# Optimization experiments

Hardware: AMD Instinct MI355X
Metric: run time of the kernel (lower is better)

Reference implementation:

```python
import jax, jax.numpy as jnp
import numpy as np

B, S, D, H = 4, 2048, 1024, 16
DK = D // H


def setup_inputs() -> dict:
    key = jax.random.key(0)
    ks = jax.random.split(key, 7)
    xq = jax.random.normal(ks[0], (B, S, D), dtype=jnp.float32)
    xk = jax.random.normal(ks[1], (B, S, D), dtype=jnp.float32)
    xv = jax.random.normal(ks[2], (B, S, D), dtype=jnp.float32)
    attention_mask = jnp.ones((B, S), dtype=jnp.int32)  # all-valid padding mask
    scale = 0.02
    Wq = jax.random.normal(ks[3], (D, D), dtype=jnp.float32) * scale
    Wk = jax.random.normal(ks[4], (D, D), dtype=jnp.float32) * scale
    Wv = jax.random.normal(ks[5], (D, D), dtype=jnp.float32) * scale
    Wo = jax.random.normal(ks[6], (D, D), dtype=jnp.float32) * scale
    return {"x_query": xq, "x_key": xk, "x_value": xv,
            "attention_mask": attention_mask,
            "Wq": Wq, "Wk": Wk, "Wv": Wv, "Wo": Wo}


def reference(x_query, x_key, x_value, attention_mask, Wq, Wk, Wv, Wo):
    b, sq, d = x_query.shape
    sk = x_key.shape[1]
    # nn.Linear(bias=False): y = x @ W.T
    Q = x_query @ Wq.T
    K = x_key @ Wk.T
    V = x_value @ Wv.T
    # torch .split(dk, dim=-1) -> contiguous head slices == reshape (B,S,H,DK)
    Qh = Q.reshape(b, sq, H, DK).transpose(0, 2, 1, 3)  # (B,H,Sq,DK)
    Kh = K.reshape(b, sk, H, DK).transpose(0, 2, 1, 3)
    Vh = V.reshape(b, sk, H, DK).transpose(0, 2, 1, 3)
    scores = jnp.einsum('bhqd,bhkd->bhqk', Qh, Kh) / jnp.sqrt(
        jnp.asarray(DK, dtype=Qh.dtype))
    # causal mask (mask_future=True)
    causal = jnp.tril(jnp.ones((sq, sk), dtype=bool))
    scores = jnp.where(causal[None, None, :, :], scores, -jnp.inf)
    # padding mask (B,Sk) -> (B,1,1,Sk)
    pad = (attention_mask != 0)[:, None, None, :]
    scores = jnp.where(pad, scores, -jnp.inf)
    attn = jax.nn.softmax(scores, axis=-1)
    out = jnp.einsum('bhqk,bhkd->bhqd', attn, Vh)  # (B,H,Sq,DK)
    out = out.transpose(0, 2, 1, 3).reshape(b, sq, d)
    return out @ Wo.T
```

## Files before the change

kernel.cpp:

```cpp
#include <hip/hip_runtime.h>
#include <stdint.h>

#define BB 4
#define SS 2048
#define DD 1024
#define HH 16
#define DKK 64

typedef unsigned short u16;
typedef short s16x8 __attribute__((ext_vector_type(8)));
typedef float f32x4 __attribute__((ext_vector_type(4)));

__device__ __forceinline__ void async_copy16(const void* g, void* l) {
  __builtin_amdgcn_global_load_lds(
      (const __attribute__((address_space(1))) void*)g,
      (__attribute__((address_space(3))) void*)l, 16, 0, 0);
}

__device__ __forceinline__ u16 f2bf(float f) {
  union { float f; uint32_t u; } x; x.f = f;
  uint32_t r = x.u + 0x7fffu + ((x.u >> 16) & 1u);
  return (u16)(r >> 16);
}

__device__ __forceinline__ uint32_t cvtpk(float a, float b) {
  uint32_t d;
  asm("v_cvt_pk_bf16_f32 %0, %1, %2" : "=v"(d) : "v"(a), "v"(b));
  return d;
}

__device__ __forceinline__ uint32_t swz16(uint32_t x) {
  return (uint32_t)__builtin_amdgcn_ds_swizzle((int)x, 0x401F);
}

__global__ __launch_bounds__(256) void cvt_kernel(
    const float* __restrict__ x0, const float* __restrict__ x1,
    const float* __restrict__ x2, const float* __restrict__ w0,
    const float* __restrict__ w1, const float* __restrict__ w2,
    const float* __restrict__ w3, u16* __restrict__ dst) {
  const size_t base = ((size_t)blockIdx.x * 256 + threadIdx.x) * 8;
  const float* src;
  size_t off;
  if (base < 25165824ull) {
    const size_t t = base >> 23;
    src = (t == 0) ? x0 : (t == 1) ? x1 : x2;
    off = base & 8388607ull;
  } else {
    const size_t r = base - 25165824ull;
    const size_t t = r >> 20;
    src = (t == 0) ? w0 : (t == 1) ? w1 : (t == 2) ? w2 : w3;
    off = r & 1048575ull;
  }
  const float4 a = *(const float4*)(src + off);
  const float4 b = *(const float4*)(src + off + 4);
  s16x8 o;
  o[0] = (short)f2bf(a.x); o[1] = (short)f2bf(a.y);
  o[2] = (short)f2bf(a.z); o[3] = (short)f2bf(a.w);
  o[4] = (short)f2bf(b.x); o[5] = (short)f2bf(b.y);
  o[6] = (short)f2bf(b.z); o[7] = (short)f2bf(b.w);
  *(s16x8*)(dst + base) = o;
}

template <bool IN_F32, bool OUT_F32>
__global__ __launch_bounds__(256, 3) void gemm_bt(
    const void* __restrict__ Ap, const void* __restrict__ Bp, void* __restrict__ Cp,
    size_t asegstride, size_t bsegstride, size_t csegstride, int vt_seg) {
  const int K = 1024, N = 1024;
  __shared__ u16 Alds[128 * 64];
  __shared__ u16 Blds[128 * 64];
  const int tid = threadIdx.x;
  const int wid = tid >> 6, lane = tid & 63;
  const int quad = lane >> 4, l16 = lane & 15;
  const int mtile = blockIdx.x >> 3;
  const int ntile = blockIdx.x & 7;
  const int wm = wid >> 1, wn = wid & 1;
  const int seg = blockIdx.y;
  f32x4 acc[4][4] = {};
  for (int kb = 0; kb < K; kb += 64) {
    if constexpr (IN_F32) {
      const float* Af = (const float*)Ap + seg * asegstride + (size_t)mtile * 128 * K;
      const float* Bf = (const float*)Bp + seg * bsegstride + (size_t)ntile * 128 * K;
#pragma unroll
      for (int i = 0; i < 8; ++i) {
        const int c = i * 256 + tid;
        const int row = c >> 4, g = c & 15;
        const int cc = g >> 1, h = g & 1;
        const int sl = row * 8 + (cc ^ (row & 7));
        {
          const float4 v = *(const float4*)(Af + (size_t)row * K + kb + g * 4);
          ushort4 o;
          o.x = f2bf(v.x); o.y = f2bf(v.y); o.z = f2bf(v.z); o.w = f2bf(v.w);
          *(ushort4*)&Alds[sl * 8 + h * 4] = o;
        }
        {
          const float4 v = *(const float4*)(Bf + (size_t)row * K + kb + g * 4);
          ushort4 o;
          o.x = f2bf(v.x); o.y = f2bf(v.y); o.z = f2bf(v.z); o.w = f2bf(v.w);
          *(ushort4*)&Blds[sl * 8 + h * 4] = o;
        }
      }
    } else {
      const u16* Ab = (const u16*)Ap + seg * asegstride + (size_t)mtile * 128 * K;
      const u16* Bb = (const u16*)Bp + seg * bsegstride + (size_t)ntile * 128 * K;
#pragma unroll
      for (int i = 0; i < 4; ++i) {
        const int s = i * 256 + tid;
        const int row = s >> 3;
        const int cc = (s & 7) ^ (row & 7);
        async_copy16(Ab + (size_t)row * K + kb + cc * 8,
                     (char*)Alds + (i * 256 + wid * 64) * 16);
        async_copy16(Bb + (size_t)row * K + kb + cc * 8,
                     (char*)Blds + (i * 256 + wid * 64) * 16);
      }
    }
    __syncthreads();
#pragma unroll
    for (int ks = 0; ks < 2; ++ks) {
      s16x8 af[4], bfr[4];
#pragma unroll
      for (int i = 0; i < 4; ++i) {
        const int R = wm * 64 + i * 16 + l16;
        af[i] = *(const s16x8*)&Alds[(R * 8 + ((ks * 4 + quad) ^ (l16 & 7))) * 8];
      }
#pragma unroll
      for (int j = 0; j < 4; ++j) {
        const int R = wn * 64 + j * 16 + l16;
        bfr[j] = *(const s16x8*)&Blds[(R * 8 + ((ks * 4 + quad) ^ (l16 & 7))) * 8];
      }
#pragma unroll
      for (int i = 0; i < 4; ++i)
#pragma unroll
        for (int j = 0; j < 4; ++j)
          acc[i][j] = __builtin_amdgcn_mfma_f32_16x16x32_bf16(af[i], bfr[j], acc[i][j], 0, 0, 0);
    }
    __syncthreads();
  }
  const int row0 = mtile * 128 + wm * 64 + quad * 4;
  const int col0 = ntile * 128 + wn * 64 + l16;
  if (seg == vt_seg) {
    u16* VT = (u16*)Cp + (size_t)seg * csegstride;
#pragma unroll
    for (int i = 0; i < 4; ++i)
#pragma unroll
      for (int j = 0; j < 4; ++j) {
        const int col = col0 + j * 16;
        const int row = row0 + i * 16;
        const int bb = row >> 11, s0 = row & 2047;
        const size_t dst = (((size_t)bb * HH + (col >> 6)) * DKK + (col & 63)) * SS + s0;
        ushort4 o;
        o.x = f2bf(acc[i][j][0]); o.y = f2bf(acc[i][j][1]);
        o.z = f2bf(acc[i][j][2]); o.w = f2bf(acc[i][j][3]);
        *(ushort4*)(VT + dst) = o;
      }
  } else {
#pragma unroll
    for (int i = 0; i < 4; ++i)
#pragma unroll
      for (int j = 0; j < 4; ++j)
#pragma unroll
        for (int r = 0; r < 4; ++r) {
          const size_t idx = (size_t)(row0 + i * 16 + r) * N + col0 + j * 16;
          if constexpr (OUT_F32) ((float*)Cp)[seg * csegstride + idx] = acc[i][j][r];
          else                   ((u16*)Cp)[seg * csegstride + idx] = f2bf(acc[i][j][r]);
        }
  }
}

__global__ __launch_bounds__(256, 4) void attn_kernel(
    const u16* __restrict__ Q, const u16* __restrict__ K, const u16* __restrict__ VT,
    const int* __restrict__ mask, u16* __restrict__ O) {
  __shared__ u16 Klds[64 * 64];
  __shared__ u16 Vt[64 * 64];
  __shared__ float bias[64];
  const int bid = blockIdx.x;
  const int qt = 15 - (bid >> 6);
  const int b = (bid >> 4) & 3;
  const int h = bid & 15;
  const int tid = threadIdx.x;
  const int wid = tid >> 6, lane = tid & 63;
  const int quad = lane >> 4, l16 = lane & 15;
  const int q0 = qt * 128;
  const u16* Qb = Q + ((size_t)b * SS + q0) * DD + h * DKK;
  const u16* Kb0 = K + (size_t)b * SS * DD + h * DKK;
  const u16* VTb = VT + ((size_t)(b * HH + h)) * DKK * SS;
  s16x8 qf[2][2];
#pragma unroll
  for (int rg = 0; rg < 2; ++rg)
#pragma unroll
    for (int ks = 0; ks < 2; ++ks)
      qf[rg][ks] = *(const s16x8*)(Qb + (size_t)(wid * 32 + rg * 16 + l16) * DD +
                                   ks * 32 + quad * 8);
  s16x8 onesf;
#pragma unroll
  for (int i = 0; i < 8; ++i) onesf[i] = (short)0x3F80;
  f32x4 oacc[2][4] = {};
  f32x4 lacc[2] = {};
  const float c_scale = 0.18033688f;
  const bool qodd = (quad & 1) != 0;
  const bool is_hi = (lane >= 32);
  const bool midq = (quad == 1) || (quad == 2);
  const int xaddr = (lane ^ 32) << 2;
  const int qrow0 = q0 + wid * 32 + l16;
  auto mixf = [&](uint32_t vj0, uint32_t vj1) -> uint32_t {
    const uint32_t S  = is_hi ? vj1 : vj0;
    const uint32_t S2 = is_hi ? vj0 : vj1;
    const uint32_t R  = (uint32_t)__builtin_amdgcn_ds_bpermute(xaddr, (int)S2);
    return midq ? R : S;
  };
  const int ktiles = 2 * qt + 2;
  for (int kt = 0; kt < ktiles; ++kt) {
    const u16* Kb = Kb0 + (size_t)(kt * 64) * DD;
#pragma unroll
    for (int i = 0; i < 2; ++i) {
      const int s = i * 256 + tid;
      const int row = s >> 3;
      const int cc = (s & 7) ^ (row & 7);
      async_copy16(Kb + (size_t)row * DD + cc * 8,
                   (char*)Klds + (i * 256 + wid * 64) * 16);
    }
#pragma unroll
    for (int i = 0; i < 2; ++i) {
      const int s = i * 256 + tid;
      const int row = s >> 3;
      const int cc = (s & 7) ^ (row & 7);
      async_copy16(VTb + (size_t)row * SS + kt * 64 + cc * 8,
                   (char*)Vt + ((i * 256 + wid * 64) * 16));
    }
    if (tid < 64) bias[tid] = mask[(size_t)b * SS + kt * 64 + tid] ? 0.0f : -1e30f;
    __syncthreads();
    f32x4 bj[4];
#pragma unroll
    for (int j = 0; j < 4; ++j) bj[j] = *(const f32x4*)&bias[j * 16 + quad * 4];
    f32x4 st[2][4] = {};
#pragma unroll
    for (int ks = 0; ks < 2; ++ks) {
      s16x8 kf[4];
#pragma unroll
      for (int j = 0; j < 4; ++j) {
        const int R = j * 16 + l16;
        kf[j] = *(const s16x8*)&Klds[(R * 8 + ((ks * 4 + quad) ^ (l16 & 7))) * 8];
      }
#pragma unroll
      for (int rg = 0; rg < 2; ++rg)
#pragma unroll
        for (int j = 0; j < 4; ++j)
          st[rg][j] = __builtin_amdgcn_mfma_f32_16x16x32_bf16(kf[j], qf[rg][ks],
                                                              st[rg][j], 0, 0, 0);
    }
    const bool causal = (kt >= 2 * qt);
    uint32_t pkv[2][8];
#pragma unroll
    for (int rg = 0; rg < 2; ++rg) {
      const int qrow = qrow0 + rg * 16;
#pragma unroll
      for (int j = 0; j < 4; ++j) {
        float p[4];
#pragma unroll
        for (int r = 0; r < 4; ++r) {
          float v = __builtin_amdgcn_exp2f(st[rg][j][r] * c_scale + bj[j][r]);
          if (causal && (kt * 64 + j * 16 + quad * 4 + r) > qrow) v = 0.0f;
          p[r] = v;
        }
        pkv[rg][j * 2 + 0] = cvtpk(p[0], p[1]);
        pkv[rg][j * 2 + 1] = cvtpk(p[2], p[3]);
      }
    }
#pragma unroll
    for (int ks = 0; ks < 2; ++ks) {
      const int j0 = ks * 2, j1 = ks * 2 + 1;
      s16x8 pf[2];
#pragma unroll
      for (int rg = 0; rg < 2; ++rg) {
        const uint32_t Xa0 = pkv[rg][j0 * 2 + 0], Xa1 = pkv[rg][j0 * 2 + 1];
        const uint32_t Xb0 = pkv[rg][j1 * 2 + 0], Xb1 = pkv[rg][j1 * 2 + 1];
        const uint32_t Pa0 = swz16(Xa0), Pa1 = swz16(Xa1);
        const uint32_t Pb0 = swz16(Xb0), Pb1 = swz16(Xb1);
        const uint32_t Ea0 = qodd ? Pa0 : Xa0, Oa0 = qodd ? Xa0 : Pa0;
        const uint32_t Ea1 = qodd ? Pa1 : Xa1, Oa1 = qodd ? Xa1 : Pa1;
        const uint32_t Eb0 = qodd ? Pb0 : Xb0, Ob0 = qodd ? Xb0 : Pb0;
        const uint32_t Eb1 = qodd ? Pb1 : Xb1, Ob1 = qodd ? Xb1 : Pb1;
        union { uint32_t w[4]; s16x8 v; } u;
        u.w[0] = mixf(Ea0, Eb0);
        u.w[1] = mixf(Ea1, Eb1);
        u.w[2] = mixf(Oa0, Ob0);
        u.w[3] = mixf(Oa1, Ob1);
        pf[rg] = u.v;
      }
#pragma unroll
      for (int jt = 0; jt < 4; ++jt) {
        const int d = jt * 16 + l16;
        const s16x8 vf = *(const s16x8*)&Vt[(d * 8 + ((ks * 4 + quad) ^ (d & 7))) * 8];
#pragma unroll
        for (int rg = 0; rg < 2; ++rg)
          oacc[rg][jt] = __builtin_amdgcn_mfma_f32_16x16x32_bf16(pf[rg], vf,
                                                                oacc[rg][jt], 0, 0, 0);
      }
#pragma unroll
      for (int rg = 0; rg < 2; ++rg)
        lacc[rg] = __builtin_amdgcn_mfma_f32_16x16x32_bf16(pf[rg], onesf, lacc[rg],
                                                           0, 0, 0);
    }
    __syncthreads();
  }
  u16* Ob = O + ((size_t)b * SS + q0) * DD + h * DKK;
#pragma unroll
  for (int rg = 0; rg < 2; ++rg)
#pragma unroll
    for (int r = 0; r < 4; ++r) {
      const float inv = 1.0f / lacc[rg][r];
      const int row = wid * 32 + rg * 16 + quad * 4 + r;
#pragma unroll
      for (int jt = 0; jt < 4; ++jt)
        Ob[(size_t)row * DD + jt * 16 + l16] = f2bf(oacc[rg][jt][r] * inv);
    }
}

extern "C" void kernel_launch(void* const* d_in, const int* in_sizes, int n_in,
                              void* d_out, int out_size, void* d_ws, size_t ws_size,
                              hipStream_t stream) {
  const float* xq = (const float*)d_in[0];
  const float* xk = (const float*)d_in[1];
  const float* xv = (const float*)d_in[2];
  const int* mask = (const int*)d_in[3];
  const float* Wq = (const float*)d_in[4];
  const float* Wk = (const float*)d_in[5];
  const float* Wv = (const float*)d_in[6];
  const float* Wo = (const float*)d_in[7];
  float* out = (float*)d_out;
  const size_t elems = (size_t)BB * SS * DD;
  const size_t welems = (size_t)DD * DD;
  if (ws_size >= 109051904ull) {
    u16* wsb = (u16*)d_ws;
    u16* Xq = wsb;
    u16* Wqb = wsb + 3 * elems;
    u16* Wob = Wqb + 3 * welems;
    u16* Qb = wsb + 3 * elems + 4 * welems;
    u16* Kb = Qb + elems;
    u16* Vb = Kb + elems;
    u16* Ob = wsb;
    cvt_kernel<<<14336, 256, 0, stream>>>(xq, xk, xv, Wq, Wk, Wv, Wo, wsb);
    gemm_bt<false, false><<<dim3(512, 3), 256, 0, stream>>>(
        Xq, Wqb, Qb, elems, welems, elems, 2);
    attn_kernel<<<BB * HH * (SS / 128), 256, 0, stream>>>(Qb, Kb, Vb, mask, Ob);
    gemm_bt<false, true><<<dim3(512, 1), 256, 0, stream>>>(Ob, Wob, out, 0, 0, 0, -1);
  } else {
    u16* Qb = (u16*)d_ws;
    u16* Kb = Qb + elems;
    u16* Vb = Kb + elems;
    u16* Ob = Vb + elems;
    gemm_bt<true, false><<<dim3(512, 1), 256, 0, stream>>>(xq, Wq, Qb, 0, 0, 0, -1);
    gemm_bt<true, false><<<dim3(512, 1), 256, 0, stream>>>(xk, Wk, Kb, 0, 0, 0, -1);
    gemm_bt<true, false><<<dim3(512, 1), 256, 0, stream>>>(xv, Wv, Vb, 0, 0, 0, 0);
    attn_kernel<<<BB * HH * (SS / 128), 256, 0, stream>>>(Qb, Kb, Vb, mask, Ob);
    gemm_bt<false, true><<<dim3(512, 1), 256, 0, stream>>>(Ob, Wo, out, 0, 0, 0, -1);
  }
}
```

Before: 318.4 us.

## Pair causal query tiles per attention block and swizzle GEMM tile order

The attention kernel now runs 512-thread blocks over 256-row query tiles. Each block handles two complementary tiles (qt and 7-qt), so every block does about the same amount of causal work, and only 256 blocks are launched. Each K/V tile loaded into LDS is shared by 8 waves instead of 4. Separately, the GEMM block index is swizzled to change the order in which M/N tiles are visited, which changes cache reuse. The trade-off is fewer, larger blocks: lower occupancy and only one wave of blocks across the CUs.

```diff
diff --git a/kernel.cpp b/kernel.cpp
--- a/kernel.cpp
+++ b/kernel.cpp
@@ -71,8 +71,10 @@
   const int tid = threadIdx.x;
   const int wid = tid >> 6, lane = tid & 63;
   const int quad = lane >> 4, l16 = lane & 15;
-  const int mtile = blockIdx.x >> 3;
-  const int ntile = blockIdx.x & 7;
+  const int bidx = blockIdx.x;
+  const int swz = ((bidx & 7) << 6) | (bidx >> 3);
+  const int mtile = swz >> 3;
+  const int ntile = swz & 7;
   const int wm = wid >> 1, wn = wid & 1;
   const int seg = blockIdx.y;
   f32x4 acc[4][4] = {};
@@ -166,153 +168,146 @@
   }
 }
 
-__global__ __launch_bounds__(256, 4) void attn_kernel(
+__global__ __launch_bounds__(512, 2) void attn_kernel(
     const u16* __restrict__ Q, const u16* __restrict__ K, const u16* __restrict__ VT,
     const int* __restrict__ mask, u16* __restrict__ O) {
   __shared__ u16 Klds[64 * 64];
   __shared__ u16 Vt[64 * 64];
   __shared__ float bias[64];
   const int bid = blockIdx.x;
-  const int qt = 15 - (bid >> 6);
+  const int pairidx = bid >> 6;
   const int b = (bid >> 4) & 3;
   const int h = bid & 15;
   const int tid = threadIdx.x;
   const int wid = tid >> 6, lane = tid & 63;
   const int quad = lane >> 4, l16 = lane & 15;
-  const int q0 = qt * 128;
-  const u16* Qb = Q + ((size_t)b * SS + q0) * DD + h * DKK;
   const u16* Kb0 = K + (size_t)b * SS * DD + h * DKK;
   const u16* VTb = VT + ((size_t)(b * HH + h)) * DKK * SS;
-  s16x8 qf[2][2];
-#pragma unroll
-  for (int rg = 0; rg < 2; ++rg)
-#pragma unroll
-    for (int ks = 0; ks < 2; ++ks)
-      qf[rg][ks] = *(const s16x8*)(Qb + (size_t)(wid * 32 + rg * 16 + l16) * DD +
-                                   ks * 32 + quad * 8);
   s16x8 onesf;
 #pragma unroll
   for (int i = 0; i < 8; ++i) onesf[i] = (short)0x3F80;
-  f32x4 oacc[2][4] = {};
-  f32x4 lacc[2] = {};
   const float c_scale = 0.18033688f;
   const bool qodd = (quad & 1) != 0;
   const bool is_hi = (lane >= 32);
   const bool midq = (quad == 1) || (quad == 2);
   const int xaddr = (lane ^ 32) << 2;
-  const int qrow0 = q0 + wid * 32 + l16;
   auto mixf = [&](uint32_t vj0, uint32_t vj1) -> uint32_t {
     const uint32_t S  = is_hi ? vj1 : vj0;
     const uint32_t S2 = is_hi ? vj0 : vj1;
     const uint32_t R  = (uint32_t)__builtin_amdgcn_ds_bpermute(xaddr, (int)S2);
     return midq ? R : S;
   };
-  const int ktiles = 2 * qt + 2;
-  for (int kt = 0; kt < ktiles; ++kt) {
-    const u16* Kb = Kb0 + (size_t)(kt * 64) * DD;
-#pragma unroll
-    for (int i = 0; i < 2; ++i) {
-      const int s = i * 256 + tid;
-      const int row = s >> 3;
-      const int cc = (s & 7) ^ (row & 7);
-      async_copy16(Kb + (size_t)row * DD + cc * 8,
-                   (char*)Klds + (i * 256 + wid * 64) * 16);
+  const int srow = tid >> 3;
+  const int scc = (tid & 7) ^ (srow & 7);
+
+  for (int half = 0; half < 2; ++half) {
+    const int qt = half ? pairidx : (7 - pairidx);
+    const int q0 = qt * 256;
+    const u16* Qb = Q + ((size_t)b * SS + q0) * DD + h * DKK;
+    s16x8 qf[2][2];
+#pragma unroll
+    for (int rg = 0; rg < 2; ++rg)
+#pragma unroll
+      for (int ks = 0; ks < 2; ++ks)
+        qf[rg][ks] = *(const s16x8*)(Qb + (size_t)(wid * 32 + rg * 16 + l16) * DD +
+                                     ks * 32 + quad * 8);
+    f32x4 oacc[2][4] = {};
+    f32x4 lacc[2] = {};
+    const int qrow0 = q0 + wid * 32 + l16;
+    const int ktiles = 4 * qt + 4;
+    for (int kt = 0; kt < ktiles; ++kt) {
+      async_copy16(Kb0 + (size_t)(kt * 64 + srow) * DD + scc * 8,
+                   (char*)Klds + wid * 1024);
+      async_copy16(VTb + (size_t)srow * SS + kt * 64 + scc * 8,
+                   (char*)Vt + wid * 1024);
+      if (tid < 64) bias[tid] = mask[(size_t)b * SS + kt * 64 + tid] ? 0.0f : -1e30f;
+      __syncthreads();
+      f32x4 bj[4];
+#pragma unroll
+      for (int j = 0; j < 4; ++j) bj[j] = *(const f32x4*)&bias[j * 16 + quad * 4];
+      f32x4 st[2][4] = {};
+#pragma unroll
+      for (int ks = 0; ks < 2; ++ks) {
+        s16x8 kf[4];
+#pragma unroll
+        for (int j = 0; j < 4; ++j) {
+          const int R = j * 16 + l16;
+          kf[j] = *(const s16x8*)&Klds[(R * 8 + ((ks * 4 + quad) ^ (l16 & 7))) * 8];
+        }
+#pragma unroll
+        for (int rg = 0; rg < 2; ++rg)
+#pragma unroll
+          for (int j = 0; j < 4; ++j)
+            st[rg][j] = __builtin_amdgcn_mfma_f32_16x16x32_bf16(kf[j], qf[rg][ks],
+                                                                st[rg][j], 0, 0, 0);
+      }
+      const bool causal = (kt >= 4 * qt);
+      uint32_t pkv[2][8];
+#pragma unroll
+      for (int rg = 0; rg < 2; ++rg) {
+        const int qrow = qrow0 + rg * 16;
+#pragma unroll
+        for (int j = 0; j < 4; ++j) {
+          float p[4];
+#pragma unroll
+          for (int r = 0; r < 4; ++r) {
+            float v = __builtin_amdgcn_exp2f(st[rg][j][r] * c_scale + bj[j][r]);
+            if (causal && (kt * 64 + j * 16 + quad * 4 + r) > qrow) v = 0.0f;
+            p[r] = v;
+          }
+          pkv[rg][j * 2 + 0] = cvtpk(p[0], p[1]);
+          pkv[rg][j * 2 + 1] = cvtpk(p[2], p[3]);
+        }
+      }
+#pragma unroll
+      for (int ks = 0; ks < 2; ++ks) {
+        const int j0 = ks * 2, j1 = ks * 2 + 1;
+        s16x8 pf[2];
+#pragma unroll
+        for (int rg = 0; rg < 2; ++rg) {
+          const uint32_t Xa0 = pkv[rg][j0 * 2 + 0], Xa1 = pkv[rg][j0 * 2 + 1];
+          const uint32_t Xb0 = pkv[rg][j1 * 2 + 0], Xb1 = pkv[rg][j1 * 2 + 1];
+          const uint32_t Pa0 = swz16(Xa0), Pa1 = swz16(Xa1);
+          const uint32_t Pb0 = swz16(Xb0), Pb1 = swz16(Xb1);
+          const uint32_t Ea0 = qodd ? Pa0 : Xa0, Oa0 = qodd ? Xa0 : Pa0;
+          const uint32_t Ea1 = qodd ? Pa1 : Xa1, Oa1 = qodd ? Xa1 : Pa1;
+          const uint32_t Eb0 = qodd ? Pb0 : Xb0, Ob0 = qodd ? Xb0 : Pb0;
+          const uint32_t Eb1 = qodd ? Pb1 : Xb1, Ob1 = qodd ? Xb1 : Pb1;
+          union { uint32_t w[4]; s16x8 v; } u;
+          u.w[0] = mixf(Ea0, Eb0);
+          u.w[1] = mixf(Ea1, Eb1);
+          u.w[2] = mixf(Oa0, Ob0);
+          u.w[3] = mixf(Oa1, Ob1);
+          pf[rg] = u.v;
+        }
+#pragma unroll
+        for (int jt = 0; jt < 4; ++jt) {
+          const int d = jt * 16 + l16;
+          const s16x8 vf = *(const s16x8*)&Vt[(d * 8 + ((ks * 4 + quad) ^ (d & 7))) * 8];
+#pragma unroll
+          for (int rg = 0; rg < 2; ++rg)
+            oacc[rg][jt] = __builtin_amdgcn_mfma_f32_16x16x32_bf16(pf[rg], vf,
+                                                                  oacc[rg][jt], 0, 0, 0);
+        }
+#pragma unroll
+        for (int rg = 0; rg < 2; ++rg)
+          lacc[rg] = __builtin_amdgcn_mfma_f32_16x16x32_bf16(pf[rg], onesf, lacc[rg],
+                                                             0, 0, 0);
+      }
+      __syncthreads();
     }
-#pragma unroll
-    for (int i = 0; i < 2; ++i) {
-      const int s = i * 256 + tid;
-      const int row = s >> 3;
-      const int cc = (s & 7) ^ (row & 7);
-      async_copy16(VTb + (size_t)row * SS + kt * 64 + cc * 8,
-                   (char*)Vt + ((i * 256 + wid * 64) * 16));
-    }
-    if (tid < 64) bias[tid] = mask[(size_t)b * SS + kt * 64 + tid] ? 0.0f : -1e30f;
-    __syncthreads();
-    f32x4 bj[4];
-#pragma unroll
-    for (int j = 0; j < 4; ++j) bj[j] = *(const f32x4*)&bias[j * 16 + quad * 4];
-    f32x4 st[2][4] = {};
-#pragma unroll
-    for (int ks = 0; ks < 2; ++ks) {
-      s16x8 kf[4];
-#pragma unroll
-      for (int j = 0; j < 4; ++j) {
-        const int R = j * 16 + l16;
-        kf[j] = *(const s16x8*)&Klds[(R * 8 + ((ks * 4 + quad) ^ (l16 & 7))) * 8];
-      }
-#pragma unroll
-      for (int rg = 0; rg < 2; ++rg)
-#pragma unroll
-        for (int j = 0; j < 4; ++j)
-          st[rg][j] = __builtin_amdgcn_mfma_f32_16x16x32_bf16(kf[j], qf[rg][ks],
-                                                              st[rg][j], 0, 0, 0);
-    }
-    const bool causal = (kt >= 2 * qt);
-    uint32_t pkv[2][8];
-#pragma unroll
-    for (int rg = 0; rg < 2; ++rg) {
-      const int qrow = qrow0 + rg * 16;
-#pragma unroll
-      for (int j = 0; j < 4; ++j) {
-        float p[4];
-#pragma unroll
-        for (int r = 0; r < 4; ++r) {
-          float v = __builtin_amdgcn_exp2f(st[rg][j][r] * c_scale + bj[j][r]);
-          if (causal && (kt * 64 + j * 16 + quad * 4 + r) > qrow) v = 0.0f;
-          p[r] = v;
-        }
-        pkv[rg][j * 2 + 0] = cvtpk(p[0], p[1]);
-        pkv[rg][j * 2 + 1] = cvtpk(p[2], p[3]);
-      }
-    }
-#pragma unroll
-    for (int ks = 0; ks < 2; ++ks) {
-      const int j0 = ks * 2, j1 = ks * 2 + 1;
-      s16x8 pf[2];
-#pragma unroll
-      for (int rg = 0; rg < 2; ++rg) {
-        const uint32_t Xa0 = pkv[rg][j0 * 2 + 0], Xa1 = pkv[rg][j0 * 2 + 1];
-        const uint32_t Xb0 = pkv[rg][j1 * 2 + 0], Xb1 = pkv[rg][j1 * 2 + 1];
-        const uint32_t Pa0 = swz16(Xa0), Pa1 = swz16(Xa1);
-        const uint32_t Pb0 = swz16(Xb0), Pb1 = swz16(Xb1);
-        const uint32_t Ea0 = qodd ? Pa0 : Xa0, Oa0 = qodd ? Xa0 : Pa0;
-        const uint32_t Ea1 = qodd ? Pa1 : Xa1, Oa1 = qodd ? Xa1 : Pa1;
-        const uint32_t Eb0 = qodd ? Pb0 : Xb0, Ob0 = qodd ? Xb0 : Pb0;
-        const uint32_t Eb1 = qodd ? Pb1 : Xb1, Ob1 = qodd ? Xb1 : Pb1;
-        union { uint32_t w[4]; s16x8 v; } u;
-        u.w[0] = mixf(Ea0, Eb0);
-        u.w[1] = mixf(Ea1, Eb1);
-        u.w[2] = mixf(Oa0, Ob0);
-        u.w[3] = mixf(Oa1, Ob1);
-        pf[rg] = u.v;
-      }
-#pragma unroll
-      for (int jt = 0; jt < 4; ++jt) {
-        const int d = jt * 16 + l16;
-        const s16x8 vf = *(const s16x8*)&Vt[(d * 8 + ((ks * 4 + quad) ^ (d & 7))) * 8];
-#pragma unroll
-        for (int rg = 0; rg < 2; ++rg)
-          oacc[rg][jt] = __builtin_amdgcn_mfma_f32_16x16x32_bf16(pf[rg], vf,
-                                                                oacc[rg][jt], 0, 0, 0);
-      }
-#pragma unroll
-      for (int rg = 0; rg < 2; ++rg)
-        lacc[rg] = __builtin_amdgcn_mfma_f32_16x16x32_bf16(pf[rg], onesf, lacc[rg],
-                                                           0, 0, 0);
-    }
-    __syncthreads();
-  }
-  u16* Ob = O + ((size_t)b * SS + q0) * DD + h * DKK;
-#pragma unroll
-  for (int rg = 0; rg < 2; ++rg)
-#pragma unroll
-    for (int r = 0; r < 4; ++r) {
-      const float inv = 1.0f / lacc[rg][r];
-      const int row = wid * 32 + rg * 16 + quad * 4 + r;
-#pragma unroll
-      for (int jt = 0; jt < 4; ++jt)
-        Ob[(size_t)row * DD + jt * 16 + l16] = f2bf(oacc[rg][jt][r] * inv);
-    }
+    u16* Ob = O + ((size_t)b * SS + q0) * DD + h * DKK;
+#pragma unroll
+    for (int rg = 0; rg < 2; ++rg)
+#pragma unroll
+      for (int r = 0; r < 4; ++r) {
+        const float inv = 1.0f / lacc[rg][r];
+        const int row = wid * 32 + rg * 16 + quad * 4 + r;
+#pragma unroll
+        for (int jt = 0; jt < 4; ++jt)
+          Ob[(size_t)row * DD + jt * 16 + l16] = f2bf(oacc[rg][jt][r] * inv);
+      }
+  }
 }
 
 extern "C" void kernel_launch(void* const* d_in, const int* in_sizes, int n_in,
@@ -341,7 +336,7 @@
     cvt_kernel<<<14336, 256, 0, stream>>>(xq, xk, xv, Wq, Wk, Wv, Wo, wsb);
     gemm_bt<false, false><<<dim3(512, 3), 256, 0, stream>>>(
         Xq, Wqb, Qb, elems, welems, elems, 2);
-    attn_kernel<<<BB * HH * (SS / 128), 256, 0, stream>>>(Qb, Kb, Vb, mask, Ob);
+    attn_kernel<<<256, 512, 0, stream>>>(Qb, Kb, Vb, mask, Ob);
     gemm_bt<false, true><<<dim3(512, 1), 256, 0, stream>>>(Ob, Wob, out, 0, 0, 0, -1);
   } else {
     u16* Qb = (u16*)d_ws;
@@ -351,7 +346,7 @@
     gemm_bt<true, false><<<dim3(512, 1), 256, 0, stream>>>(xq, Wq, Qb, 0, 0, 0, -1);
     gemm_bt<true, false><<<dim3(512, 1), 256, 0, stream>>>(xk, Wk, Kb, 0, 0, 0, -1);
     gemm_bt<true, false><<<dim3(512, 1), 256, 0, stream>>>(xv, Wv, Vb, 0, 0, 0, 0);
-    attn_kernel<<<BB * HH * (SS / 128), 256, 0, stream>>>(Qb, Kb, Vb, mask, Ob);
+    attn_kernel<<<256, 512, 0, stream>>>(Qb, Kb, Vb, mask, Ob);
     gemm_bt<false, true><<<dim3(512, 1), 256, 0, stream>>>(Ob, Wo, out, 0, 0, 0, -1);
   }
 }
```

After: 324.3 us. No clear change (+1.9%).

## Split long causal attention tiles across two blocks and add combine kernel

Applied to the files above, without the earlier changes.

The causal attention launch gets a split-K mode. The eight longest query tiles per (batch, head) are split into two halves over the key range, each writing fp32 partial outputs and row sums, and a new combine kernel merges them. The block-to-tile mapping is a hard-coded schedule meant to balance work across the 1536 blocks. This targets the load imbalance from causal triangles and adds extra fp32 traffic plus one more launch. The GEMM block index is also swizzled, changing the order in which tiles are visited for cache locality.

```diff
diff --git a/kernel.cpp b/kernel.cpp
--- a/kernel.cpp
+++ b/kernel.cpp
@@ -71,8 +71,10 @@
   const int tid = threadIdx.x;
   const int wid = tid >> 6, lane = tid & 63;
   const int quad = lane >> 4, l16 = lane & 15;
-  const int mtile = blockIdx.x >> 3;
-  const int ntile = blockIdx.x & 7;
+  const int bidx = blockIdx.x;
+  const int swz = ((bidx & 7) << 6) | (bidx >> 3);
+  const int mtile = swz >> 3;
+  const int ntile = swz & 7;
   const int wm = wid >> 1, wn = wid & 1;
   const int seg = blockIdx.y;
   f32x4 acc[4][4] = {};
@@ -166,16 +168,35 @@
   }
 }
 
+template <int MODE>
 __global__ __launch_bounds__(256, 4) void attn_kernel(
     const u16* __restrict__ Q, const u16* __restrict__ K, const u16* __restrict__ VT,
-    const int* __restrict__ mask, u16* __restrict__ O) {
+    const int* __restrict__ mask, u16* __restrict__ O,
+    float* __restrict__ Opart, float* __restrict__ lpart) {
   __shared__ u16 Klds[64 * 64];
   __shared__ u16 Vt[64 * 64];
   __shared__ float bias[64];
   const int bid = blockIdx.x;
-  const int qt = 15 - (bid >> 6);
-  const int b = (bid >> 4) & 3;
-  const int h = bid & 15;
+  int qt, kt0, kt1, code, bh;
+  if constexpr (MODE == 0) {
+    qt = 15 - (bid >> 6);
+    bh = bid & 63;
+    code = 2;
+    kt0 = 0; kt1 = 2 * qt + 2;
+  } else {
+    bh = bid & 63;
+    const int w = bid >> 6;
+    const int wsel = w >> 3, wo = w & 7;
+    const uint32_t qw = (wsel == 0) ? 0xDD6EE7FFu : (wsel == 1) ? 0x4AABB5CCu : 0x01238899u;
+    const uint32_t sw = (wsel == 0) ? 0x4924u : (wsel == 1) ? 0x9124u : 0xAA44u;
+    qt = (int)((qw >> (wo * 4)) & 15u);
+    code = (int)((sw >> (wo * 2)) & 3u);
+    const int half = qt + 1;
+    kt0 = (code == 1) ? half : 0;
+    kt1 = (code == 0) ? half : 2 * qt + 2;
+  }
+  const int b = bh >> 4;
+  const int h = bh & 15;
   const int tid = threadIdx.x;
   const int wid = tid >> 6, lane = tid & 63;
   const int quad = lane >> 4, l16 = lane & 15;
@@ -207,8 +228,7 @@
     const uint32_t R  = (uint32_t)__builtin_amdgcn_ds_bpermute(xaddr, (int)S2);
     return midq ? R : S;
   };
-  const int ktiles = 2 * qt + 2;
-  for (int kt = 0; kt < ktiles; ++kt) {
+  for (int kt = kt0; kt < kt1; ++kt) {
     const u16* Kb = Kb0 + (size_t)(kt * 64) * DD;
 #pragma unroll
     for (int i = 0; i < 2; ++i) {
@@ -302,17 +322,61 @@
     }
     __syncthreads();
   }
-  u16* Ob = O + ((size_t)b * SS + q0) * DD + h * DKK;
-#pragma unroll
-  for (int rg = 0; rg < 2; ++rg)
-#pragma unroll
-    for (int r = 0; r < 4; ++r) {
-      const float inv = 1.0f / lacc[rg][r];
-      const int row = wid * 32 + rg * 16 + quad * 4 + r;
-#pragma unroll
-      for (int jt = 0; jt < 4; ++jt)
-        Ob[(size_t)row * DD + jt * 16 + l16] = f2bf(oacc[rg][jt][r] * inv);
-    }
+  if (code == 2) {
+    u16* Ob = O + ((size_t)b * SS + q0) * DD + h * DKK;
+#pragma unroll
+    for (int rg = 0; rg < 2; ++rg)
+#pragma unroll
+      for (int r = 0; r < 4; ++r) {
+        const float inv = 1.0f / lacc[rg][r];
+        const int row = wid * 32 + rg * 16 + quad * 4 + r;
+#pragma unroll
+        for (int jt = 0; jt < 4; ++jt)
+          Ob[(size_t)row * DD + jt * 16 + l16] = f2bf(oacc[rg][jt][r] * inv);
+      }
+  } else {
+    const int tile = (bh << 3) + (qt - 8);
+    const int p = tile * 2 + code;
+    float* Op = Opart + (size_t)p * 8192;
+    float* lp = lpart + (size_t)p * 128;
+#pragma unroll
+    for (int rg = 0; rg < 2; ++rg)
+#pragma unroll
+      for (int r = 0; r < 4; ++r) {
+        const int row = wid * 32 + rg * 16 + quad * 4 + r;
+        if (l16 == 0) lp[row] = lacc[rg][r];
+#pragma unroll
+        for (int jt = 0; jt < 4; ++jt)
+          Op[row * 64 + jt * 16 + l16] = oacc[rg][jt][r];
+      }
+  }
+}
+
+__global__ __launch_bounds__(256) void combine_kernel(
+    const float* __restrict__ Opart, const float* __restrict__ lpart,
+    u16* __restrict__ O) {
+  const int tile = blockIdx.x;
+  const int bh = tile >> 3;
+  const int qt = (tile & 7) + 8;
+  const int b = bh >> 4, h = bh & 15;
+  const int tid = threadIdx.x;
+  const int row = tid >> 1;
+  const int c0 = (tid & 1) * 32;
+  const float* P0 = Opart + ((size_t)tile * 2 + 0) * 8192 + row * 64 + c0;
+  const float* P1 = Opart + ((size_t)tile * 2 + 1) * 8192 + row * 64 + c0;
+  const float l = lpart[((size_t)tile * 2 + 0) * 128 + row] +
+                  lpart[((size_t)tile * 2 + 1) * 128 + row];
+  const float inv = 1.0f / l;
+  u16* Ob = O + ((size_t)b * SS + qt * 128 + row) * DD + h * DKK + c0;
+#pragma unroll
+  for (int i = 0; i < 8; ++i) {
+    const f32x4 a = *(const f32x4*)(P0 + i * 4);
+    const f32x4 c = *(const f32x4*)(P1 + i * 4);
+    ushort4 o;
+    o.x = f2bf((a[0] + c[0]) * inv); o.y = f2bf((a[1] + c[1]) * inv);
+    o.z = f2bf((a[2] + c[2]) * inv); o.w = f2bf((a[3] + c[3]) * inv);
+    *(ushort4*)(Ob + i * 4) = o;
+  }
 }
 
 extern "C" void kernel_launch(void* const* d_in, const int* in_sizes, int n_in,
@@ -338,10 +402,13 @@
     u16* Kb = Qb + elems;
     u16* Vb = Kb + elems;
     u16* Ob = wsb;
+    float* Opart = (float*)(wsb + elems);
+    float* lpart = (float*)(wsb + 3 * elems);
     cvt_kernel<<<14336, 256, 0, stream>>>(xq, xk, xv, Wq, Wk, Wv, Wo, wsb);
     gemm_bt<false, false><<<dim3(512, 3), 256, 0, stream>>>(
         Xq, Wqb, Qb, elems, welems, elems, 2);
-    attn_kernel<<<BB * HH * (SS / 128), 256, 0, stream>>>(Qb, Kb, Vb, mask, Ob);
+    attn_kernel<1><<<1536, 256, 0, stream>>>(Qb, Kb, Vb, mask, Ob, Opart, lpart);
+    combine_kernel<<<512, 256, 0, stream>>>(Opart, lpart, Ob);
     gemm_bt<false, true><<<dim3(512, 1), 256, 0, stream>>>(Ob, Wob, out, 0, 0, 0, -1);
   } else {
     u16* Qb = (u16*)d_ws;
@@ -351,7 +418,8 @@
     gemm_bt<true, false><<<dim3(512, 1), 256, 0, stream>>>(xq, Wq, Qb, 0, 0, 0, -1);
     gemm_bt<true, false><<<dim3(512, 1), 256, 0, stream>>>(xk, Wk, Kb, 0, 0, 0, -1);
     gemm_bt<true, false><<<dim3(512, 1), 256, 0, stream>>>(xv, Wv, Vb, 0, 0, 0, 0);
-    attn_kernel<<<BB * HH * (SS / 128), 256, 0, stream>>>(Qb, Kb, Vb, mask, Ob);
+    attn_kernel<0><<<1024, 256, 0, stream>>>(Qb, Kb, Vb, mask, Ob,
+                                             (float*)d_ws, (float*)d_ws);
     gemm_bt<false, true><<<dim3(512, 1), 256, 0, stream>>>(Ob, Wo, out, 0, 0, 0, -1);
   }
 }
```

New measurement: 314.8 us. Within noise of the previous version (-1.1%).
